# Optimization experiments

Measured on AMD Instinct MI355X. Metric: run time of the kernel, lower is better.

## Reference

```python
import jax, jax.numpy as jnp
import numpy as np

L = 4          # decoder layers (model_config "[4,[0],0]")
D = 1024       # d_model
H = 16         # n_head
DH = 64        # d_head
DI = 4096      # d_inner
V = 16000      # n_token (add_eot=False)
S = 1024       # seq len
B = 4          # batch
EPS = 1e-5


def _layer_norm(x, g, b):
    mu = jnp.mean(x, axis=-1, keepdims=True)
    var = jnp.mean(jnp.square(x - mu), axis=-1, keepdims=True)
    return (x - mu) * jax.lax.rsqrt(var + EPS) * g + b


def _rel_shift(x):
    # x: [b, n, q, k]
    b, n, q, k = x.shape
    zero_pad = jnp.zeros((b, n, q, 1), dtype=x.dtype)
    xp = jnp.concatenate([zero_pad, x], axis=3)        # [b,n,q,k+1]
    xp = xp.reshape(b, n, k + 1, q)
    return xp[:, :, 1:, :].reshape(b, n, q, k)


def setup_inputs() -> dict:
    key = jax.random.key(0)
    ks = list(jax.random.split(key, 24))
    sd = 0.02
    inp = {}
    inp["tokens"] = jax.random.randint(ks[0], (S, B), 0, V)
    inp["word_emb"] = jax.random.normal(ks[1], (V, D), jnp.float32) * sd
    inp["r_w_bias"] = jax.random.normal(ks[2], (H, DH), jnp.float32) * sd
    inp["r_r_bias"] = jax.random.normal(ks[3], (H, DH), jnp.float32) * sd
    inp["qkv_w"] = jax.random.normal(ks[4], (L, D, 3 * H * DH), jnp.float32) * sd
    inp["qkv_b"] = jnp.zeros((L, 3 * H * DH), jnp.float32)
    inp["r_kw"] = jax.random.normal(ks[5], (L, D, H * DH), jnp.float32) * sd
    inp["r_kb"] = jnp.zeros((L, H * DH), jnp.float32)
    inp["o_w"] = jax.random.normal(ks[6], (L, H * DH, D), jnp.float32) * sd
    inp["o_b"] = jnp.zeros((L, D), jnp.float32)
    inp["ln1_g"] = jnp.ones((L, D), jnp.float32)
    inp["ln1_b"] = jnp.zeros((L, D), jnp.float32)
    inp["ff1_w"] = jax.random.normal(ks[7], (L, D, DI), jnp.float32) * sd
    inp["ff1_b"] = jnp.zeros((L, DI), jnp.float32)
    inp["ff2_w"] = jax.random.normal(ks[8], (L, DI, D), jnp.float32) * sd
    inp["ff2_b"] = jnp.zeros((L, D), jnp.float32)
    inp["ln2_g"] = jnp.ones((L, D), jnp.float32)
    inp["ln2_b"] = jnp.zeros((L, D), jnp.float32)
    inp["final_w"] = jax.random.normal(ks[9], (D, V), jnp.float32) * sd
    inp["final_b"] = jnp.zeros((V,), jnp.float32)
    return inp


def reference(tokens, word_emb, r_w_bias, r_r_bias, qkv_w, qkv_b, r_kw, r_kb,
              o_w, o_b, ln1_g, ln1_b, ff1_w, ff1_b, ff2_w, ff2_b,
              ln2_g, ln2_b, final_w, final_b):
    s, b = tokens.shape
    h = word_emb[tokens]                                 # [S,B,D]
    # sinusoidal relative positions, pos_seq = klen-1 ... 0
    pos_seq = jnp.arange(s - 1, -1, -1, dtype=h.dtype)
    inv_freq = 1.0 / (10000.0 ** (jnp.arange(0, D, 2, dtype=h.dtype) / D))
    sinu = pos_seq[:, None] * inv_freq[None, :]
    r = jnp.concatenate([jnp.sin(sinu), jnp.cos(sinu)], axis=-1)   # [S,D]
    # causal mask: True = masked (j > i)
    mask = jnp.triu(jnp.ones((s, s), dtype=bool), k=1)
    scale = 1.0 / (DH ** 0.5)
    neg_inf = jnp.asarray(-jnp.inf, dtype=h.dtype)

    for l in range(L):
        qkv = h @ qkv_w[l] + qkv_b[l]                    # [S,B,3*H*DH]
        q, k, v = jnp.split(qkv, 3, axis=-1)
        q = q.reshape(s, b, H, DH)
        k = k.reshape(s, b, H, DH)
        v = v.reshape(s, b, H, DH)
        rk = (r @ r_kw[l] + r_kb[l]).reshape(s, H, DH)   # [S,H,DH]
        AC = jnp.einsum('ibnd,jbnd->bnij', q + r_w_bias, k)
        BD = jnp.einsum('ibnd,jnd->bnij', q + r_r_bias, rk)
        BD = _rel_shift(BD)
        score = scale * (AC + BD)
        score = jnp.where(mask[None, None, :, :], neg_inf, score)
        prob = jax.nn.softmax(score, axis=-1)
        vec = jnp.einsum('bnij,jbnd->ibnd', prob, v).reshape(s, b, H * DH)
        attn_out = vec @ o_w[l] + o_b[l]
        h = _layer_norm(h + attn_out, ln1_g[l], ln1_b[l])
        ff = jax.nn.gelu(h @ ff1_w[l] + ff1_b[l], approximate=False) @ ff2_w[l] + ff2_b[l]
        h = _layer_norm(h + ff, ln2_g[l], ln2_b[l])

    logits = h @ final_w + final_b                       # [S,B,V]
    return logits
```

## Files before the change

### kernel.cpp

```cpp
#include <hip/hip_runtime.h>

#define S 1024
#define Bb 4
#define Hh 16
#define DHh 64
#define Dm 1024
#define DIi 4096
#define Vv 16000
#define Lll 4

typedef __attribute__((ext_vector_type(4))) float f32x4;
typedef __attribute__((ext_vector_type(8))) __bf16 bf16x8;
typedef __attribute__((ext_vector_type(8))) unsigned short u16x8;
typedef __attribute__((ext_vector_type(4))) unsigned short u16x4;

__device__ __forceinline__ unsigned short f2bf(float f) {
  unsigned int u = __float_as_uint(f);
  u += 0x7fffu + ((u >> 16) & 1u);
  return (unsigned short)(u >> 16);
}
__device__ __forceinline__ float bf2f(unsigned short u) {
  return __uint_as_float(((unsigned int)u) << 16);
}

__device__ __forceinline__ void gload_lds16(const void* g, void* l) {
  __builtin_amdgcn_global_load_lds((const __attribute__((address_space(1))) unsigned int*)g,
                                   (__attribute__((address_space(3))) unsigned int*)l, 16, 0, 0);
}

__device__ __forceinline__ f32x4 mfma_bf16(bf16x8 a, bf16x8 b, f32x4 c) {
  return __builtin_amdgcn_mfma_f32_16x16x32_bf16(a, b, c, 0, 0, 0);
}

__global__ __launch_bounds__(256) void embed_k(const int* __restrict__ tokens,
                                               const float* __restrict__ we,
                                               float* __restrict__ h,
                                               unsigned short* __restrict__ hb) {
  int row = blockIdx.x;
  int t = threadIdx.x;
  int tok = tokens[row];
  f32x4 v = *(const f32x4*)&we[(long)tok * Dm + t * 4];
  *(f32x4*)&h[(long)row * Dm + t * 4] = v;
  u16x4 r;
#pragma unroll
  for (int e = 0; e < 4; ++e) r[e] = f2bf(v[e]);
  *(u16x4*)&hb[(long)row * Dm + t * 4] = r;
}

__global__ __launch_bounds__(256) void posr_k(unsigned short* __restrict__ r) {
  int idx = blockIdx.x * 256 + threadIdx.x;
  int u = idx >> 10, d = idx & 1023;
  float pos = (float)(S - 1 - u);
  int j = d & 511;
  float invf = powf(10000.0f, -(float)j * (1.0f / 512.0f));
  float a = pos * invf;
  r[idx] = f2bf(d < 512 ? sinf(a) : cosf(a));
}

__global__ __launch_bounds__(256) void wcvt_t(const float* __restrict__ W,
                                              unsigned short* __restrict__ WT,
                                              int Kd, int Nd) {
  __shared__ unsigned short tile[32][40];
  int n0 = blockIdx.x * 32, k0 = blockIdx.y * 32;
  const float* Wb = W + (long)blockIdx.z * Kd * Nd;
  unsigned short* WTb = WT + (long)blockIdx.z * Kd * Nd;
  int t = threadIdx.x;
  int rr = t >> 3, c4 = (t & 7) * 4;
  f32x4 v = *(const f32x4*)&Wb[(long)(k0 + rr) * Nd + n0 + c4];
#pragma unroll
  for (int e = 0; e < 4; ++e) tile[rr][c4 + e] = f2bf(v[e]);
  __syncthreads();
  if (t < 128) {
    int n = t >> 2, k8 = (t & 3) * 8;
    u16x8 pk;
#pragma unroll
    for (int e = 0; e < 8; ++e) pk[e] = tile[k8 + e][n];
    *(u16x8*)&WTb[(long)(n0 + n) * Kd + k0 + k8] = pk;
  }
}

template <int EPI>
__global__ __launch_bounds__(256) void gemm_bt(const unsigned short* __restrict__ A,
                                               const unsigned short* __restrict__ BT,
                                               const float* __restrict__ bias,
                                               void* __restrict__ Cout,
                                               int M, int N, int K, int ntn) {
  __shared__ unsigned short As[128 * 64];
  __shared__ unsigned short Bs[128 * 64];
  const int tid = threadIdx.x;
  const int lane = tid & 63;
  const int w = tid >> 6;
  const int nwg = gridDim.x;
  const int qq = nwg >> 3, rr = nwg & 7;
  const int xcd = blockIdx.x & 7, loc = blockIdx.x >> 3;
  const int wg = (xcd < rr ? xcd * (qq + 1) : rr * (qq + 1) + (xcd - rr) * qq) + loc;
  const int bn = (wg % ntn) * 128, bm = (wg / ntn) * 128;
  const int wr = (w >> 1) * 64, wc = (w & 1) * 64;
  const int la = lane & 15, lk = (lane >> 4) * 8;
  f32x4 acc[4][4] = {};

  const int rrow = tid >> 3;
  const int rcol = (tid & 7) * 8;
  const unsigned short* ag = A + (long)(bm + rrow) * K + rcol;
  const unsigned short* bg = BT + (long)(bn + rrow) * K + rcol;

  for (int k0 = 0; k0 < K; k0 += 64) {
    __syncthreads();
#pragma unroll
    for (int c = 0; c < 4; ++c) {
      gload_lds16(ag + (long)c * 32 * K + k0, &As[c * 2048 + w * 512]);
      gload_lds16(bg + (long)c * 32 * K + k0, &Bs[c * 2048 + w * 512]);
    }
    __syncthreads();
#pragma unroll
    for (int kk = 0; kk < 2; ++kk) {
      bf16x8 af[4], bq[4];
#pragma unroll
      for (int mi = 0; mi < 4; ++mi)
        af[mi] = *(const bf16x8*)&As[(wr + mi * 16 + la) * 64 + kk * 32 + lk];
#pragma unroll
      for (int ni = 0; ni < 4; ++ni)
        bq[ni] = *(const bf16x8*)&Bs[(wc + ni * 16 + la) * 64 + kk * 32 + lk];
#pragma unroll
      for (int mi = 0; mi < 4; ++mi)
#pragma unroll
        for (int ni = 0; ni < 4; ++ni)
          acc[mi][ni] = mfma_bf16(af[mi], bq[ni], acc[mi][ni]);
    }
  }
  const int cr = (lane >> 4) * 4;
#pragma unroll
  for (int mi = 0; mi < 4; ++mi) {
#pragma unroll
    for (int ni = 0; ni < 4; ++ni) {
      int col = bn + wc + ni * 16 + la;
      float bv = bias[col];
      int row = bm + wr + mi * 16 + cr;
#pragma unroll
      for (int e = 0; e < 4; ++e) {
        float v = acc[mi][ni][e] + bv;
        if (EPI == 0) {
          ((float*)Cout)[(long)(row + e) * N + col] = v;
        } else if (EPI == 1) {
          ((unsigned short*)Cout)[(long)(row + e) * N + col] = f2bf(v);
        } else {
          float g = 0.5f * v * (1.0f + erff(v * 0.70710678118f));
          ((unsigned short*)Cout)[(long)(row + e) * N + col] = f2bf(g);
        }
      }
    }
  }
}

__global__ __launch_bounds__(256) void qkv_prep(const unsigned short* __restrict__ q3,
                                                const float* __restrict__ rwb,
                                                const float* __restrict__ rrb,
                                                unsigned short* __restrict__ qw,
                                                unsigned short* __restrict__ qr,
                                                unsigned short* __restrict__ kb) {
  int idx = blockIdx.x * 256 + threadIdx.x;
  int c8 = (idx & 127) * 8;
  int row = idx >> 7;
  int s = row >> 2, b = row & 3;
  int n = c8 >> 6, d = c8 & 63;
  u16x8 qv = *(const u16x8*)&q3[(long)row * 3072 + c8];
  u16x8 kv = *(const u16x8*)&q3[(long)row * 3072 + 1024 + c8];
  long o = ((long)(b * Hh + n) * S + s) * 64 + d;
  u16x8 ow, orr;
#pragma unroll
  for (int e = 0; e < 8; ++e) {
    float q = bf2f(qv[e]);
    ow[e] = f2bf(q + rwb[c8 + e]);
    orr[e] = f2bf(q + rrb[c8 + e]);
  }
  *(u16x8*)&qw[o] = ow;
  *(u16x8*)&qr[o] = orr;
  *(u16x8*)&kb[o] = kv;
}

__global__ __launch_bounds__(256) void vt_prep(const unsigned short* __restrict__ q3,
                                               unsigned short* __restrict__ vT) {
  __shared__ unsigned short tile[64][72];
  const int it = blockIdx.x, bn = blockIdx.y;
  const int nh = bn & 15, bbv = bn >> 4;
  const int t = threadIdx.x;
  const int i0 = t >> 3, c8 = (t & 7) * 8;
#pragma unroll
  for (int c = 0; c < 2; ++c) {
    int i = i0 + c * 32;
    u16x8 v = *(const u16x8*)&q3[((long)(it * 64 + i) * Bb + bbv) * 3072 + 2048 + nh * 64 + c8];
    *(u16x8*)&tile[i][c8] = v;
  }
  __syncthreads();
  for (int cc = t; cc < 512; cc += 256) {
    int d = cc >> 3, i8 = (cc & 7) * 8;
    u16x8 pk;
#pragma unroll
    for (int e = 0; e < 8; ++e) pk[e] = tile[i8 + e][d];
    *(u16x8*)&vT[((long)bn * 64 + d) * S + it * 64 + i8] = pk;
  }
}

__global__ __launch_bounds__(256) void rkb_prep(const unsigned short* __restrict__ rkall,
                                                unsigned short* __restrict__ rkb) {
  int idx = blockIdx.x * 256 + threadIdx.x;
  int d8 = (idx & 7) * 8;
  int u = (idx >> 3) & 1023;
  int nl = idx >> 13;
  int l = nl >> 4, n = nl & 15;
  u16x8 v = *(const u16x8*)&rkall[(long)u * 4096 + l * 1024 + n * 64 + d8];
  *(u16x8*)&rkb[(long)idx * 8] = v;
}

__global__ __launch_bounds__(256) void attn_k(const unsigned short* __restrict__ qw,
                                              const unsigned short* __restrict__ qr,
                                              const unsigned short* __restrict__ kbuf,
                                              const unsigned short* __restrict__ vT,
                                              const unsigned short* __restrict__ rk,
                                              unsigned short* __restrict__ vec) {
  __shared__ unsigned short Ks[2][64 * 64];
  __shared__ unsigned short Vs[2][64 * 64];
  __shared__ unsigned short plds[4][16][72];
  const int tid = threadIdx.x, lane = tid & 63, w = tid >> 6;
  const int bn = blockIdx.x >> 3, pr = blockIdx.x & 7;
  const int nh = bn & 15, bbv = bn >> 4;
  const int la = lane & 15, hi = lane >> 4, lk = hi * 8;
  const int hi4 = hi * 4;
  const unsigned short* kbase = kbuf + (long)bn * S * 64;
  const unsigned short* vbase = vT + (long)bn * 64 * S;
  const unsigned short* rbase = rk + (long)nh * S * 64;

  const int q0 = w * 128 + lane;
  const int r0 = q0 >> 3, c0s = (q0 & 7) ^ (r0 & 7);
  const int q1 = q0 + 64;
  const int r1 = q1 >> 3, c1s = (q1 & 7) ^ (r1 & 7);

  int cur = 0;
#pragma unroll 1
  for (int half = 0; half < 2; ++half) {
    const int it = half ? (15 - pr) : pr;
    const int iw = it * 64 + w * 16;
    bf16x8 qwf[2], qrf[2];
    {
      const unsigned short* qp = qw + ((long)bn * S + iw + la) * 64 + lk;
      qwf[0] = *(const bf16x8*)qp;
      qwf[1] = *(const bf16x8*)(qp + 32);
      const unsigned short* qp2 = qr + ((long)bn * S + iw + la) * 64 + lk;
      qrf[0] = *(const bf16x8*)qp2;
      qrf[1] = *(const bf16x8*)(qp2 + 32);
    }
    f32x4 opv[4] = {};
    float m_[4] = {-3e38f, -3e38f, -3e38f, -3e38f};
    float l_[4] = {0.f, 0.f, 0.f, 0.f};

    gload_lds16(kbase + (long)r0 * 64 + c0s * 8, &Ks[cur][w * 1024]);
    gload_lds16(kbase + (long)r1 * 64 + c1s * 8, &Ks[cur][w * 1024 + 512]);
    gload_lds16(vbase + (long)r0 * S + c0s * 8, &Vs[cur][w * 1024]);
    gload_lds16(vbase + (long)r1 * S + c1s * 8, &Vs[cur][w * 1024 + 512]);
    __syncthreads();

    for (int jt = 0; jt <= it; ++jt) {
      const int j0 = jt * 64;
      const bool edge = (jt == it);
      if (jt < it) {
        const int jn = j0 + 64;
        gload_lds16(kbase + (long)(jn + r0) * 64 + c0s * 8, &Ks[cur ^ 1][w * 1024]);
        gload_lds16(kbase + (long)(jn + r1) * 64 + c1s * 8, &Ks[cur ^ 1][w * 1024 + 512]);
        gload_lds16(vbase + (long)r0 * S + jn + c0s * 8, &Vs[cur ^ 1][w * 1024]);
        gload_lds16(vbase + (long)r1 * S + jn + c1s * 8, &Vs[cur ^ 1][w * 1024 + 512]);
      }
      const int u0 = S - 16 - iw + j0;
      bf16x8 rf[10];
#pragma unroll
      for (int g = 0; g < 5; ++g) {
        int u = u0 + g * 16 + la;
        if (edge) u = (u > S - 1) ? (S - 1) : u;
        const unsigned short* rp = rbase + (long)u * 64 + lk;
        rf[2 * g] = *(const bf16x8*)rp;
        rf[2 * g + 1] = *(const bf16x8*)(rp + 32);
      }
      f32x4 ac[4] = {};
#pragma unroll
      for (int f = 0; f < 4; ++f) {
        int row = f * 16 + la;
        const unsigned short* kl = &Ks[cur][row * 64];
        bf16x8 k0 = *(const bf16x8*)(kl + (((hi) ^ (row & 7)) << 3));
        bf16x8 k1 = *(const bf16x8*)(kl + (((hi + 4) ^ (row & 7)) << 3));
        ac[f] = mfma_bf16(qwf[0], k0, ac[f]);
        ac[f] = mfma_bf16(qwf[1], k1, ac[f]);
      }
      f32x4 gg[5] = {};
#pragma unroll
      for (int g = 0; g < 5; ++g) {
        gg[g] = mfma_bf16(qrf[0], rf[2 * g], gg[g]);
        gg[g] = mfma_bf16(qrf[1], rf[2 * g + 1], gg[g]);
      }
      float p[4][4];
#pragma unroll
      for (int f = 0; f < 4; ++f) {
#pragma unroll
        for (int e = 0; e < 4; ++e) {
          int r = hi4 + e;
          float x = (la >= 15 - r) ? gg[f][e] : gg[f + 1][e];
          int src = (lane & 48) | ((la + 15 - r) & 15);
          float bd = __shfl(x, src, 64);
          float sc = (ac[f][e] + bd) * 0.125f;
          if (edge) {
            int i_ = iw + r, j_ = j0 + f * 16 + la;
            sc = (j_ > i_) ? -1e30f : sc;
          }
          p[f][e] = sc;
        }
      }
#pragma unroll
      for (int e = 0; e < 4; ++e) {
        float mx = fmaxf(fmaxf(p[0][e], p[1][e]), fmaxf(p[2][e], p[3][e]));
#pragma unroll
        for (int o = 1; o < 16; o <<= 1) mx = fmaxf(mx, __shfl_xor(mx, o, 64));
        float mnew = fmaxf(m_[e], mx);
        float alpha = __expf(m_[e] - mnew);
        m_[e] = mnew;
        float rs = 0.f;
#pragma unroll
        for (int f = 0; f < 4; ++f) {
          p[f][e] = __expf(p[f][e] - mnew);
          rs += p[f][e];
        }
        l_[e] = l_[e] * alpha + rs;
#pragma unroll
        for (int d = 0; d < 4; ++d) opv[d][e] *= alpha;
      }
#pragma unroll
      for (int f = 0; f < 4; ++f)
#pragma unroll
        for (int e = 0; e < 4; ++e)
          plds[w][hi4 + e][f * 16 + la] = f2bf(p[f][e]);
      bf16x8 pa0 = *(const bf16x8*)&plds[w][la][lk];
      bf16x8 pa1 = *(const bf16x8*)&plds[w][la][32 + lk];
#pragma unroll
      for (int d = 0; d < 4; ++d) {
        int dd = d * 16 + la;
        const unsigned short* vl = &Vs[cur][dd * 64];
        bf16x8 v0 = *(const bf16x8*)(vl + (((hi) ^ (dd & 7)) << 3));
        bf16x8 v1 = *(const bf16x8*)(vl + (((hi + 4) ^ (dd & 7)) << 3));
        opv[d] = mfma_bf16(pa0, v0, opv[d]);
        opv[d] = mfma_bf16(pa1, v1, opv[d]);
      }
      __syncthreads();
      if (jt < it) cur ^= 1;
    }
#pragma unroll
    for (int e = 0; e < 4; ++e) {
#pragma unroll
      for (int o = 1; o < 16; o <<= 1) l_[e] += __shfl_xor(l_[e], o, 64);
    }
#pragma unroll
    for (int d = 0; d < 4; ++d) {
#pragma unroll
      for (int e = 0; e < 4; ++e) {
        int i_ = iw + hi4 + e;
        int col = nh * 64 + d * 16 + la;
        vec[((long)i_ * Bb + bbv) * 1024 + col] = f2bf(opv[d][e] / l_[e]);
      }
    }
  }
}

__global__ __launch_bounds__(256) void add_ln(float* __restrict__ h, const float* __restrict__ x,
                                              const float* __restrict__ g, const float* __restrict__ b,
                                              unsigned short* __restrict__ hb) {
  __shared__ float red[8];
  int row = blockIdx.x, t = threadIdx.x;
  long base = (long)row * 1024 + t * 4;
  f32x4 hv = *(const f32x4*)&h[base];
  f32x4 xv = *(const f32x4*)&x[base];
  f32x4 y = hv + xv;
  float s = y[0] + y[1] + y[2] + y[3];
  float q = y[0] * y[0] + y[1] * y[1] + y[2] * y[2] + y[3] * y[3];
#pragma unroll
  for (int o = 1; o < 64; o <<= 1) {
    s += __shfl_xor(s, o, 64);
    q += __shfl_xor(q, o, 64);
  }
  int w = t >> 6, lane = t & 63;
  if (lane == 0) { red[w] = s; red[4 + w] = q; }
  __syncthreads();
  s = red[0] + red[1] + red[2] + red[3];
  q = red[4] + red[5] + red[6] + red[7];
  float mu = s * (1.0f / 1024.0f);
  float var = q * (1.0f / 1024.0f) - mu * mu;
  float rstd = rsqrtf(var + 1e-5f);
  f32x4 gv = *(const f32x4*)&g[t * 4];
  f32x4 bv = *(const f32x4*)&b[t * 4];
  f32x4 o;
  u16x4 ob;
#pragma unroll
  for (int e = 0; e < 4; ++e) {
    o[e] = (y[e] - mu) * rstd * gv[e] + bv[e];
    ob[e] = f2bf(o[e]);
  }
  *(f32x4*)&h[base] = o;
  *(u16x4*)&hb[base] = ob;
}

extern "C" void kernel_launch(void* const* d_in, const int* in_sizes, int n_in,
                              void* d_out, int out_size, void* d_ws, size_t ws_size,
                              hipStream_t stream) {
  const int* tokens = (const int*)d_in[0];
  const float* word_emb = (const float*)d_in[1];
  const float* rwb = (const float*)d_in[2];
  const float* rrb = (const float*)d_in[3];
  const float* qkv_w = (const float*)d_in[4];
  const float* qkv_b = (const float*)d_in[5];
  const float* r_kw = (const float*)d_in[6];
  const float* r_kb = (const float*)d_in[7];
  const float* o_w = (const float*)d_in[8];
  const float* o_b = (const float*)d_in[9];
  const float* ln1g = (const float*)d_in[10];
  const float* ln1b = (const float*)d_in[11];
  const float* ff1w = (const float*)d_in[12];
  const float* ff1b = (const float*)d_in[13];
  const float* ff2w = (const float*)d_in[14];
  const float* ff2b = (const float*)d_in[15];
  const float* ln2g = (const float*)d_in[16];
  const float* ln2b = (const float*)d_in[17];
  const float* fw = (const float*)d_in[18];
  const float* fb = (const float*)d_in[19];

  char* ws = (char*)d_ws;
  unsigned short* WBF = (unsigned short*)(ws);
  float* H = (float*)(ws + 33554432);
  unsigned short* HB = (unsigned short*)(ws + 50331648);
  unsigned short* GB = (unsigned short*)(ws + 58720256);
  unsigned short* RBF = (unsigned short*)(ws + 92274688);

  char* ob = (char*)d_out;
  float* OUTF = (float*)ob;
  unsigned short* OUTH = (unsigned short*)ob;
  unsigned short* QW = (unsigned short*)(ob + 67108864);
  unsigned short* QR = (unsigned short*)(ob + 75497472);
  unsigned short* KB = (unsigned short*)(ob + 83886080);
  unsigned short* VT = (unsigned short*)(ob + 92274688);
  unsigned short* RKB = (unsigned short*)(ob + 100663296);
  float* OUT = (float*)d_out;

  embed_k<<<4096, 256, 0, stream>>>(tokens, word_emb, H, HB);
  posr_k<<<4096, 256, 0, stream>>>(RBF);
  wcvt_t<<<dim3(32, 32, 4), 256, 0, stream>>>(r_kw, WBF, 1024, 1024);
  gemm_bt<1><<<256, 256, 0, stream>>>(RBF, WBF, r_kb, OUTH, 1024, 4096, 1024, 32);
  rkb_prep<<<2048, 256, 0, stream>>>(OUTH, RKB);

  for (int l = 0; l < Lll; ++l) {
    wcvt_t<<<dim3(96, 32, 1), 256, 0, stream>>>(qkv_w + (long)l * 1024 * 3072, WBF, 1024, 3072);
    gemm_bt<1><<<768, 256, 0, stream>>>(HB, WBF, qkv_b + l * 3072, OUTH, 4096, 3072, 1024, 24);
    qkv_prep<<<2048, 256, 0, stream>>>(OUTH, rwb, rrb, QW, QR, KB);
    vt_prep<<<dim3(16, 64), 256, 0, stream>>>(OUTH, VT);
    attn_k<<<512, 256, 0, stream>>>(QW, QR, KB, VT, RKB + (long)l * Hh * S * 64, HB);
    wcvt_t<<<dim3(32, 32, 1), 256, 0, stream>>>(o_w + (long)l * 1024 * 1024, WBF, 1024, 1024);
    gemm_bt<0><<<256, 256, 0, stream>>>(HB, WBF, o_b + l * 1024, OUTF, 4096, 1024, 1024, 8);
    add_ln<<<4096, 256, 0, stream>>>(H, OUTF, ln1g + l * 1024, ln1b + l * 1024, HB);

    wcvt_t<<<dim3(128, 32, 1), 256, 0, stream>>>(ff1w + (long)l * 1024 * 4096, WBF, 1024, 4096);
    gemm_bt<2><<<1024, 256, 0, stream>>>(HB, WBF, ff1b + l * 4096, GB, 4096, 4096, 1024, 32);
    wcvt_t<<<dim3(32, 128, 1), 256, 0, stream>>>(ff2w + (long)l * 4096 * 1024, WBF, 4096, 1024);
    gemm_bt<0><<<256, 256, 0, stream>>>(GB, WBF, ff2b + l * 1024, OUTF, 4096, 1024, 4096, 8);
    add_ln<<<4096, 256, 0, stream>>>(H, OUTF, ln2g + l * 1024, ln2b + l * 1024, HB);
  }

  wcvt_t<<<dim3(500, 32, 1), 256, 0, stream>>>(fw, WBF, 1024, 16000);
  gemm_bt<0><<<4000, 256, 0, stream>>>(HB, WBF, fb, OUT, 4096, 16000, 1024, 125);
}
```

Before: 1.700 ms.

## Swizzle GEMM LDS layout, add M-major tile order, lazy softmax rescale

Replaces the GEMM kernel with a variant whose LDS staging uses a permuted layout so MFMA fragment reads avoid bank conflicts, adds occupancy launch bounds and an optional M-major tile ordering used for the vocab projection. Pads the final projection to a multiple of 128 columns with bounds checks. In attention, switches to a single per-row-group running max and only rescales the accumulators when the new max exceeds the old by more than a threshold, which cuts exp and multiply work. The lazy rescale relies on bounded exponent growth and could affect numerics in extreme cases.

```diff
diff --git a/kernel.cpp b/kernel.cpp
--- a/kernel.cpp
+++ b/kernel.cpp
@@ -62,11 +62,13 @@
                                               int Kd, int Nd) {
   __shared__ unsigned short tile[32][40];
   int n0 = blockIdx.x * 32, k0 = blockIdx.y * 32;
+  const bool inb = n0 < Nd;
   const float* Wb = W + (long)blockIdx.z * Kd * Nd;
   unsigned short* WTb = WT + (long)blockIdx.z * Kd * Nd;
   int t = threadIdx.x;
   int rr = t >> 3, c4 = (t & 7) * 4;
-  f32x4 v = *(const f32x4*)&Wb[(long)(k0 + rr) * Nd + n0 + c4];
+  f32x4 v = {0.f, 0.f, 0.f, 0.f};
+  if (inb) v = *(const f32x4*)&Wb[(long)(k0 + rr) * Nd + n0 + c4];
 #pragma unroll
   for (int e = 0; e < 4; ++e) tile[rr][c4 + e] = f2bf(v[e]);
   __syncthreads();
@@ -80,72 +82,72 @@
 }
 
 template <int EPI>
-__global__ __launch_bounds__(256) void gemm_bt(const unsigned short* __restrict__ A,
-                                               const unsigned short* __restrict__ BT,
-                                               const float* __restrict__ bias,
-                                               void* __restrict__ Cout,
-                                               int M, int N, int K, int ntn) {
-  __shared__ unsigned short As[128 * 64];
-  __shared__ unsigned short Bs[128 * 64];
-  const int tid = threadIdx.x;
-  const int lane = tid & 63;
-  const int w = tid >> 6;
+__global__ __launch_bounds__(256, 4) void gemm_f(
+    const unsigned short* __restrict__ A, const unsigned short* __restrict__ BT,
+    const float* __restrict__ bias, void* __restrict__ Cout,
+    int M, int N, int K, int ntm, int ntn, int morder) {
+  __shared__ unsigned short As[8192];
+  __shared__ unsigned short Bs[8192];
+  const int tid = threadIdx.x, lane = tid & 63, w = tid >> 6;
+  const int la = lane & 15, hi = lane >> 4;
   const int nwg = gridDim.x;
   const int qq = nwg >> 3, rr = nwg & 7;
   const int xcd = blockIdx.x & 7, loc = blockIdx.x >> 3;
   const int wg = (xcd < rr ? xcd * (qq + 1) : rr * (qq + 1) + (xcd - rr) * qq) + loc;
-  const int bn = (wg % ntn) * 128, bm = (wg / ntn) * 128;
-  const int wr = (w >> 1) * 64, wc = (w & 1) * 64;
-  const int la = lane & 15, lk = (lane >> 4) * 8;
+  int bm, bn;
+  if (morder) { bm = (wg % ntm) * 128; bn = (wg / ntm) * 128; }
+  else        { bn = (wg % ntn) * 128; bm = (wg / ntn) * 128; }
+  const int wr = w >> 1, wc = w & 1;
   f32x4 acc[4][4] = {};
 
-  const int rrow = tid >> 3;
-  const int rcol = (tid & 7) * 8;
-  const unsigned short* ag = A + (long)(bm + rrow) * K + rcol;
-  const unsigned short* bg = BT + (long)(bn + rrow) * K + rcol;
+  const unsigned short* srcA = A + (long)(bm + (w >> 1) * 16 + la) * K + ((w * 4 + hi) & 7) * 8;
+  const unsigned short* srcB = BT + (long)(bn + (w >> 1) * 16 + la) * K + ((w * 4 + hi) & 7) * 8;
+  const long cstep = (long)32 * K;
+  const unsigned short* Ard = As + wr * 4096 + hi * 128 + la * 8;
+  const unsigned short* Brd = Bs + wc * 4096 + hi * 128 + la * 8;
 
   for (int k0 = 0; k0 < K; k0 += 64) {
     __syncthreads();
 #pragma unroll
     for (int c = 0; c < 4; ++c) {
-      gload_lds16(ag + (long)c * 32 * K + k0, &As[c * 2048 + w * 512]);
-      gload_lds16(bg + (long)c * 32 * K + k0, &Bs[c * 2048 + w * 512]);
+      gload_lds16(srcA + k0 + c * cstep, &As[c * 2048 + w * 512]);
+      gload_lds16(srcB + k0 + c * cstep, &Bs[c * 2048 + w * 512]);
     }
     __syncthreads();
 #pragma unroll
     for (int kk = 0; kk < 2; ++kk) {
       bf16x8 af[4], bq[4];
 #pragma unroll
-      for (int mi = 0; mi < 4; ++mi)
-        af[mi] = *(const bf16x8*)&As[(wr + mi * 16 + la) * 64 + kk * 32 + lk];
-#pragma unroll
-      for (int ni = 0; ni < 4; ++ni)
-        bq[ni] = *(const bf16x8*)&Bs[(wc + ni * 16 + la) * 64 + kk * 32 + lk];
-#pragma unroll
-      for (int mi = 0; mi < 4; ++mi)
-#pragma unroll
-        for (int ni = 0; ni < 4; ++ni)
-          acc[mi][ni] = mfma_bf16(af[mi], bq[ni], acc[mi][ni]);
-    }
-  }
-  const int cr = (lane >> 4) * 4;
-#pragma unroll
-  for (int mi = 0; mi < 4; ++mi) {
-#pragma unroll
-    for (int ni = 0; ni < 4; ++ni) {
-      int col = bn + wc + ni * 16 + la;
-      float bv = bias[col];
-      int row = bm + wr + mi * 16 + cr;
-#pragma unroll
-      for (int e = 0; e < 4; ++e) {
-        float v = acc[mi][ni][e] + bv;
-        if (EPI == 0) {
-          ((float*)Cout)[(long)(row + e) * N + col] = v;
-        } else if (EPI == 1) {
-          ((unsigned short*)Cout)[(long)(row + e) * N + col] = f2bf(v);
-        } else {
-          float g = 0.5f * v * (1.0f + erff(v * 0.70710678118f));
-          ((unsigned short*)Cout)[(long)(row + e) * N + col] = f2bf(g);
+      for (int m = 0; m < 4; ++m) af[m] = *(const bf16x8*)(Ard + m * 1024 + kk * 512);
+#pragma unroll
+      for (int n = 0; n < 4; ++n) bq[n] = *(const bf16x8*)(Brd + n * 1024 + kk * 512);
+#pragma unroll
+      for (int m = 0; m < 4; ++m)
+#pragma unroll
+        for (int n = 0; n < 4; ++n)
+          acc[m][n] = mfma_bf16(af[m], bq[n], acc[m][n]);
+    }
+  }
+
+#pragma unroll
+  for (int m = 0; m < 4; ++m) {
+#pragma unroll
+    for (int n = 0; n < 4; ++n) {
+      int col = bn + wc * 64 + n * 16 + la;
+      if (col < N) {
+        float bv = bias[col];
+        int row = bm + wr * 64 + m * 16 + hi * 4;
+#pragma unroll
+        for (int e = 0; e < 4; ++e) {
+          float v = acc[m][n][e] + bv;
+          if (EPI == 0) {
+            ((float*)Cout)[(long)(row + e) * N + col] = v;
+          } else if (EPI == 1) {
+            ((unsigned short*)Cout)[(long)(row + e) * N + col] = f2bf(v);
+          } else {
+            float g = 0.5f * v * (1.0f + erff(v * 0.70710678118f));
+            ((unsigned short*)Cout)[(long)(row + e) * N + col] = f2bf(g);
+          }
         }
       }
     }
@@ -250,7 +252,7 @@
       qrf[1] = *(const bf16x8*)(qp2 + 32);
     }
     f32x4 opv[4] = {};
-    float m_[4] = {-3e38f, -3e38f, -3e38f, -3e38f};
+    float m_ = -3e38f;
     float l_[4] = {0.f, 0.f, 0.f, 0.f};
 
     gload_lds16(kbase + (long)r0 * 64 + c0s * 8, &Ks[cur][w * 1024]);
@@ -312,23 +314,33 @@
           p[f][e] = sc;
         }
       }
+      float mx = p[0][0];
+#pragma unroll
+      for (int f = 0; f < 4; ++f)
+#pragma unroll
+        for (int e = 0; e < 4; ++e) mx = fmaxf(mx, p[f][e]);
+#pragma unroll
+      for (int o = 1; o < 16; o <<= 1) mx = fmaxf(mx, __shfl_xor(mx, o, 64));
+      if (!__all(mx <= m_ + 8.0f)) {
+        float mnew = fmaxf(m_, mx);
+        float alpha = __expf(m_ - mnew);
+        m_ = mnew;
+#pragma unroll
+        for (int e = 0; e < 4; ++e) l_[e] *= alpha;
+#pragma unroll
+        for (int d = 0; d < 4; ++d)
+#pragma unroll
+          for (int e = 0; e < 4; ++e) opv[d][e] *= alpha;
+      }
 #pragma unroll
       for (int e = 0; e < 4; ++e) {
-        float mx = fmaxf(fmaxf(p[0][e], p[1][e]), fmaxf(p[2][e], p[3][e]));
-#pragma unroll
-        for (int o = 1; o < 16; o <<= 1) mx = fmaxf(mx, __shfl_xor(mx, o, 64));
-        float mnew = fmaxf(m_[e], mx);
-        float alpha = __expf(m_[e] - mnew);
-        m_[e] = mnew;
         float rs = 0.f;
 #pragma unroll
         for (int f = 0; f < 4; ++f) {
-          p[f][e] = __expf(p[f][e] - mnew);
+          p[f][e] = __expf(p[f][e] - m_);
           rs += p[f][e];
         }
-        l_[e] = l_[e] * alpha + rs;
-#pragma unroll
-        for (int d = 0; d < 4; ++d) opv[d][e] *= alpha;
+        l_[e] += rs;
       }
 #pragma unroll
       for (int f = 0; f < 4; ++f)
@@ -447,26 +459,26 @@
   embed_k<<<4096, 256, 0, stream>>>(tokens, word_emb, H, HB);
   posr_k<<<4096, 256, 0, stream>>>(RBF);
   wcvt_t<<<dim3(32, 32, 4), 256, 0, stream>>>(r_kw, WBF, 1024, 1024);
-  gemm_bt<1><<<256, 256, 0, stream>>>(RBF, WBF, r_kb, OUTH, 1024, 4096, 1024, 32);
+  gemm_f<1><<<256, 256, 0, stream>>>(RBF, WBF, r_kb, OUTH, 1024, 4096, 1024, 8, 32, 0);
   rkb_prep<<<2048, 256, 0, stream>>>(OUTH, RKB);
 
   for (int l = 0; l < Lll; ++l) {
     wcvt_t<<<dim3(96, 32, 1), 256, 0, stream>>>(qkv_w + (long)l * 1024 * 3072, WBF, 1024, 3072);
-    gemm_bt<1><<<768, 256, 0, stream>>>(HB, WBF, qkv_b + l * 3072, OUTH, 4096, 3072, 1024, 24);
+    gemm_f<1><<<768, 256, 0, stream>>>(HB, WBF, qkv_b + l * 3072, OUTH, 4096, 3072, 1024, 32, 24, 0);
     qkv_prep<<<2048, 256, 0, stream>>>(OUTH, rwb, rrb, QW, QR, KB);
     vt_prep<<<dim3(16, 64), 256, 0, stream>>>(OUTH, VT);
     attn_k<<<512, 256, 0, stream>>>(QW, QR, KB, VT, RKB + (long)l * Hh * S * 64, HB);
     wcvt_t<<<dim3(32, 32, 1), 256, 0, stream>>>(o_w + (long)l * 1024 * 1024, WBF, 1024, 1024);
-    gemm_bt<0><<<256, 256, 0, stream>>>(HB, WBF, o_b + l * 1024, OUTF, 4096, 1024, 1024, 8);
+    gemm_f<0><<<256, 256, 0, stream>>>(HB, WBF, o_b + l * 1024, OUTF, 4096, 1024, 1024, 32, 8, 0);
     add_ln<<<4096, 256, 0, stream>>>(H, OUTF, ln1g + l * 1024, ln1b + l * 1024, HB);
 
     wcvt_t<<<dim3(128, 32, 1), 256, 0, stream>>>(ff1w + (long)l * 1024 * 4096, WBF, 1024, 4096);
-    gemm_bt<2><<<1024, 256, 0, stream>>>(HB, WBF, ff1b + l * 4096, GB, 4096, 4096, 1024, 32);
+    gemm_f<2><<<1024, 256, 0, stream>>>(HB, WBF, ff1b + l * 4096, GB, 4096, 4096, 1024, 32, 32, 0);
     wcvt_t<<<dim3(32, 128, 1), 256, 0, stream>>>(ff2w + (long)l * 4096 * 1024, WBF, 4096, 1024);
-    gemm_bt<0><<<256, 256, 0, stream>>>(GB, WBF, ff2b + l * 1024, OUTF, 4096, 1024, 4096, 8);
+    gemm_f<0><<<256, 256, 0, stream>>>(GB, WBF, ff2b + l * 1024, OUTF, 4096, 1024, 4096, 32, 8, 0);
     add_ln<<<4096, 256, 0, stream>>>(H, OUTF, ln2g + l * 1024, ln2b + l * 1024, HB);
   }
 
-  wcvt_t<<<dim3(500, 32, 1), 256, 0, stream>>>(fw, WBF, 1024, 16000);
-  gemm_bt<0><<<4000, 256, 0, stream>>>(HB, WBF, fb, OUT, 4096, 16000, 1024, 125);
-}
+  wcvt_t<<<dim3(504, 32, 1), 256, 0, stream>>>(fw, WBF, 1024, 16000);
+  gemm_f<0><<<4032, 256, 0, stream>>>(HB, WBF, fb, OUT, 4096, 16000, 1024, 32, 126, 1);
+}
```

Measured after the change: 1.899 ms. +11.7%, slower.
